# Performance work log

Hardware: AMD Instinct MI355X
Metric: run time of the kernel (lower is better)

Reference implementation:

```python
import jax, jax.numpy as jnp
import numpy as np

T, V, D = 16, 1024, 128  # number_steps, number_vectors, latent_dimension
B = 2048
EPS = 1e-12  # tf.nn.l2_normalize epsilon


def _l2_normalize(x, axis=-1):
    sq = jnp.sum(jnp.square(x), axis=axis, keepdims=True)
    return x * jax.lax.rsqrt(jnp.maximum(sq, EPS))


def setup_inputs() -> dict:
    key = jax.random.key(0)
    k1, k2, k3 = jax.random.split(key, 3)
    inputs = jax.random.normal(k1, (B, D, 1), dtype=jnp.float32)
    index = jax.random.randint(k2, (B,), 0, T, dtype=jnp.int64)
    # glorot_uniform over (T, V, D): limit = sqrt(6 / (fan_in + fan_out))
    limit = float(np.sqrt(6.0 / (V + D)))
    latent_vectors = jax.random.uniform(k3, (T, V, D), minval=-limit, maxval=limit, dtype=jnp.float32)
    return {"inputs": inputs, "latent_vectors": latent_vectors, "index": index}


def reference(inputs, latent_vectors, index):
    x = jnp.squeeze(inputs, axis=-1)                 # (B, D)
    cur = latent_vectors[index]                      # (B, V, D) gather over steps
    xn = _l2_normalize(x, axis=-1)                   # (B, D)
    ln = _l2_normalize(cur, axis=-1)                 # (B, V, D)
    sim = jnp.einsum('bvd,bd->bv', ln, xn)           # cosine similarity (B, V)
    best = jnp.argmax(sim, axis=-1)                  # (B,)
    sel = jnp.take_along_axis(cur, best[:, None, None], axis=1)  # (B, 1, D)
    return jnp.squeeze(sel, axis=1)                  # (B, D)
```

## Files before the change

### kernel.cpp

```cpp
#include <hip/hip_runtime.h>
#include <cstdint>

#define T_STEPS 16
#define V_VECS  1024
#define D_DIM   128
#define B_BATCH 2048
#define BCAP    2048

__global__ __launch_bounds__(256) void k_score(const float* __restrict__ X,
                                               const float* __restrict__ L,
                                               const int* __restrict__ idx,
                                               unsigned long long* __restrict__ partial,
                                               int* __restrict__ counts) {
    __shared__ __align__(16) float As[D_DIM][64];
    __shared__ __align__(16) float Xs[D_DIM][64];
    __shared__ float npart[4][64];
    __shared__ float invn_s[64];
    __shared__ int   blist[BCAP];
    __shared__ int   wcnt[4];

    const int t    = blockIdx.y;
    const int vt   = blockIdx.x;
    const int v0   = vt * 64;
    const int z    = blockIdx.z;
    const int tid  = threadIdx.x;
    const int lane = tid & 63;
    const int w    = tid >> 6;

    int nbase = 0;
    for (int r = 0; r < 8; ++r) {
        const int b = r * 256 + tid;
        const bool m = (idx[b] == t);
        const unsigned long long bal = __ballot(m);
        const int wpre = __popcll(bal & ((1ull << lane) - 1ull));
        if (lane == 0) wcnt[w] = __popcll(bal);
        __syncthreads();
        const int c0 = wcnt[0], c1 = wcnt[1], c2 = wcnt[2], c3 = wcnt[3];
        int base = nbase;
        if (w > 0) base += c0;
        if (w > 1) base += c1;
        if (w > 2) base += c2;
        if (m) blist[base + wpre] = b;
        nbase += c0 + c1 + c2 + c3;
        __syncthreads();
    }
    const int n = nbase;
    if (vt == 0 && z == 0 && tid == 0) counts[t] = n;
    if (z * 64 >= n) return;

    const float4* LA = (const float4*)(L + (size_t)(t * V_VECS + v0) * D_DIM);
    float ss = 0.f;
    #pragma unroll
    for (int p = 0; p < 8; ++p) {
        const int k4 = w + 4 * p;
        const float4 g = LA[lane * 32 + k4];
        As[4 * k4 + 0][lane] = g.x;
        As[4 * k4 + 1][lane] = g.y;
        As[4 * k4 + 2][lane] = g.z;
        As[4 * k4 + 3][lane] = g.w;
        ss += g.x * g.x + g.y * g.y + g.z * g.z + g.w * g.w;
    }
    npart[w][lane] = ss;
    __syncthreads();
    if (tid < 64) {
        const float s = npart[0][tid] + npart[1][tid] + npart[2][tid] + npart[3][tid];
        invn_s[tid] = rsqrtf(fmaxf(s, 1e-12f));
    }

    const int tv = tid & 15;
    const int tb = tid >> 4;
    const float4* XA = (const float4*)X;

    for (int cs = z * 64; cs < n; cs += 128) {
        __syncthreads();

        const int brow = cs + lane;
        const int bg = (brow < n) ? blist[brow] : -1;
        #pragma unroll
        for (int p = 0; p < 8; ++p) {
            const int k4 = w + 4 * p;
            float4 g = make_float4(0.f, 0.f, 0.f, 0.f);
            if (bg >= 0) g = XA[bg * 32 + k4];
            Xs[4 * k4 + 0][lane] = g.x;
            Xs[4 * k4 + 1][lane] = g.y;
            Xs[4 * k4 + 2][lane] = g.z;
            Xs[4 * k4 + 3][lane] = g.w;
        }
        __syncthreads();

        float acc[4][4] = {};
        #pragma unroll 16
        for (int k = 0; k < D_DIM; ++k) {
            const float4 av = *(const float4*)&As[k][tv * 4];
            const float4 xb = *(const float4*)&Xs[k][tb * 4];
            const float a[4] = {av.x, av.y, av.z, av.w};
            const float x[4] = {xb.x, xb.y, xb.z, xb.w};
            #pragma unroll
            for (int i = 0; i < 4; ++i)
                #pragma unroll
                for (int j = 0; j < 4; ++j)
                    acc[i][j] += a[i] * x[j];
        }

        const float invp[4] = {invn_s[tv * 4 + 0], invn_s[tv * 4 + 1],
                               invn_s[tv * 4 + 2], invn_s[tv * 4 + 3]};

        #pragma unroll
        for (int j = 0; j < 4; ++j) {
            float s = acc[0][j] * invp[0];
            int   c = v0 + tv * 4;
            #pragma unroll
            for (int i = 1; i < 4; ++i) {
                const float si = acc[i][j] * invp[i];
                const int   ci = v0 + tv * 4 + i;
                if (si > s) { s = si; c = ci; }
            }
            #pragma unroll
            for (int m = 8; m >= 1; m >>= 1) {
                const float u  = __shfl_xor(s, m);
                const int   cu = __shfl_xor(c, m);
                if (u > s || (u == s && cu < c)) { s = u; c = cu; }
            }
            if (tv == 0) {
                const int bi = cs + tb * 4 + j;
                if (bi < n) {
                    unsigned int ub = __float_as_uint(s);
                    ub = (ub & 0x80000000u) ? ~ub : (ub | 0x80000000u);
                    const unsigned long long key =
                        ((unsigned long long)ub << 32) |
                        ((unsigned long long)(unsigned)(1023 - c) << 16) |
                        (unsigned long long)(unsigned)blist[bi];
                    partial[((size_t)vt * T_STEPS + t) * BCAP + bi] = key;
                }
            }
        }
    }
}

__global__ __launch_bounds__(256) void k_gather(const float* __restrict__ L,
                                                const int* __restrict__ counts,
                                                const unsigned long long* __restrict__ partial,
                                                float* __restrict__ out) {
    __shared__ int vArr[64];
    __shared__ int bArr[64];

    const int t  = blockIdx.y;
    const int cs = blockIdx.x * 64;
    const int n  = counts[t];
    if (cs >= n) return;

    const int tid = threadIdx.x;
    const int nb  = min(64, n - cs);
    if (tid < nb) {
        const int bi = cs + tid;
        unsigned long long best = partial[(size_t)t * BCAP + bi];
        #pragma unroll
        for (int q = 1; q < 16; ++q) {
            const unsigned long long k2 =
                partial[((size_t)q * T_STEPS + t) * BCAP + bi];
            if (k2 > best) best = k2;
        }
        vArr[tid] = 1023 - (int)((best >> 16) & 0xffffull);
        bArr[tid] = (int)(best & 0xffffull);
    }
    __syncthreads();

    const int l32 = tid & 31;
    for (int q = tid >> 5; q < nb; q += 8) {
        const int b = bArr[q], v = vArr[q];
        ((float4*)out)[b * 32 + l32] =
            ((const float4*)L)[(size_t)(t * V_VECS + v) * 32 + l32];
    }
}

extern "C" void kernel_launch(void* const* d_in, const int* in_sizes, int n_in,
                              void* d_out, int out_size, void* d_ws, size_t ws_size,
                              hipStream_t stream) {
    const float* X  = (const float*)d_in[0];
    const float* L  = (const float*)d_in[1];
    const int* idx  = (const int*)d_in[2];
    float* out      = (float*)d_out;

    char* ws = (char*)d_ws;
    int* counts               = (int*)ws;
    unsigned long long* part  = (unsigned long long*)(ws + 4096);

    hipLaunchKernelGGL(k_score,  dim3(16, 16, 2), dim3(256), 0, stream,
                       X, L, idx, part, counts);
    hipLaunchKernelGGL(k_gather, dim3(32, 16),    dim3(256), 0, stream,
                       L, counts, part, out);
}
```

Measured before the change: 28.34 us.

## Shrink score kernel to single-wave blocks with 8x8 register tiles

```diff
diff --git a/kernel.cpp b/kernel.cpp
--- a/kernel.cpp
+++ b/kernel.cpp
@@ -7,122 +7,105 @@
 #define B_BATCH 2048
 #define BCAP    2048
 
-__global__ __launch_bounds__(256) void k_score(const float* __restrict__ X,
-                                               const float* __restrict__ L,
-                                               const int* __restrict__ idx,
-                                               unsigned long long* __restrict__ partial,
-                                               int* __restrict__ counts) {
+__global__ __launch_bounds__(64) void k_score(const float* __restrict__ X,
+                                              const float* __restrict__ L,
+                                              const int* __restrict__ idx,
+                                              unsigned long long* __restrict__ partial,
+                                              int* __restrict__ counts) {
     __shared__ __align__(16) float As[D_DIM][64];
     __shared__ __align__(16) float Xs[D_DIM][64];
-    __shared__ float npart[4][64];
     __shared__ float invn_s[64];
     __shared__ int   blist[BCAP];
-    __shared__ int   wcnt[4];
 
     const int t    = blockIdx.y;
     const int vt   = blockIdx.x;
     const int v0   = vt * 64;
     const int z    = blockIdx.z;
-    const int tid  = threadIdx.x;
-    const int lane = tid & 63;
-    const int w    = tid >> 6;
+    const int lane = threadIdx.x;
 
-    int nbase = 0;
-    for (int r = 0; r < 8; ++r) {
-        const int b = r * 256 + tid;
+    int n = 0;
+    for (int r = 0; r < 32; ++r) {
+        const int b = r * 64 + lane;
         const bool m = (idx[b] == t);
         const unsigned long long bal = __ballot(m);
-        const int wpre = __popcll(bal & ((1ull << lane) - 1ull));
-        if (lane == 0) wcnt[w] = __popcll(bal);
-        __syncthreads();
-        const int c0 = wcnt[0], c1 = wcnt[1], c2 = wcnt[2], c3 = wcnt[3];
-        int base = nbase;
-        if (w > 0) base += c0;
-        if (w > 1) base += c1;
-        if (w > 2) base += c2;
-        if (m) blist[base + wpre] = b;
-        nbase += c0 + c1 + c2 + c3;
-        __syncthreads();
+        if (m) blist[n + __popcll(bal & ((1ull << lane) - 1ull))] = b;
+        n += __popcll(bal);
     }
-    const int n = nbase;
-    if (vt == 0 && z == 0 && tid == 0) counts[t] = n;
+    if (vt == 0 && z == 0 && lane == 0) counts[t] = n;
     if (z * 64 >= n) return;
 
     const float4* LA = (const float4*)(L + (size_t)(t * V_VECS + v0) * D_DIM);
     float ss = 0.f;
-    #pragma unroll
-    for (int p = 0; p < 8; ++p) {
-        const int k4 = w + 4 * p;
-        const float4 g = LA[lane * 32 + k4];
-        As[4 * k4 + 0][lane] = g.x;
-        As[4 * k4 + 1][lane] = g.y;
-        As[4 * k4 + 2][lane] = g.z;
-        As[4 * k4 + 3][lane] = g.w;
+    #pragma unroll 8
+    for (int p = 0; p < 32; ++p) {
+        const float4 g = LA[lane * 32 + p];
+        As[4 * p + 0][lane] = g.x;
+        As[4 * p + 1][lane] = g.y;
+        As[4 * p + 2][lane] = g.z;
+        As[4 * p + 3][lane] = g.w;
         ss += g.x * g.x + g.y * g.y + g.z * g.z + g.w * g.w;
     }
-    npart[w][lane] = ss;
-    __syncthreads();
-    if (tid < 64) {
-        const float s = npart[0][tid] + npart[1][tid] + npart[2][tid] + npart[3][tid];
-        invn_s[tid] = rsqrtf(fmaxf(s, 1e-12f));
-    }
+    invn_s[lane] = rsqrtf(fmaxf(ss, 1e-12f));
 
-    const int tv = tid & 15;
-    const int tb = tid >> 4;
+    const int iv = lane & 7;
+    const int jb = lane >> 3;
     const float4* XA = (const float4*)X;
 
     for (int cs = z * 64; cs < n; cs += 128) {
         __syncthreads();
 
-        const int brow = cs + lane;
-        const int bg = (brow < n) ? blist[brow] : -1;
-        #pragma unroll
-        for (int p = 0; p < 8; ++p) {
-            const int k4 = w + 4 * p;
+        const int bl = cs + lane;
+        const int bg = (bl < n) ? blist[bl] : -1;
+        const float4* xr = XA + (size_t)(bg < 0 ? 0 : bg) * 32;
+        #pragma unroll 8
+        for (int p = 0; p < 32; ++p) {
             float4 g = make_float4(0.f, 0.f, 0.f, 0.f);
-            if (bg >= 0) g = XA[bg * 32 + k4];
-            Xs[4 * k4 + 0][lane] = g.x;
-            Xs[4 * k4 + 1][lane] = g.y;
-            Xs[4 * k4 + 2][lane] = g.z;
-            Xs[4 * k4 + 3][lane] = g.w;
+            if (bg >= 0) g = xr[p];
+            Xs[4 * p + 0][lane] = g.x;
+            Xs[4 * p + 1][lane] = g.y;
+            Xs[4 * p + 2][lane] = g.z;
+            Xs[4 * p + 3][lane] = g.w;
         }
         __syncthreads();
 
-        float acc[4][4] = {};
-        #pragma unroll 16
+        float acc[8][8] = {};
+        #pragma unroll 4
         for (int k = 0; k < D_DIM; ++k) {
-            const float4 av = *(const float4*)&As[k][tv * 4];
-            const float4 xb = *(const float4*)&Xs[k][tb * 4];
-            const float a[4] = {av.x, av.y, av.z, av.w};
-            const float x[4] = {xb.x, xb.y, xb.z, xb.w};
+            const float4 a0 = *(const float4*)&As[k][iv * 8];
+            const float4 a1 = *(const float4*)&As[k][iv * 8 + 4];
+            const float4 x0 = *(const float4*)&Xs[k][jb * 8];
+            const float4 x1 = *(const float4*)&Xs[k][jb * 8 + 4];
+            const float a[8] = {a0.x, a0.y, a0.z, a0.w, a1.x, a1.y, a1.z, a1.w};
+            const float x[8] = {x0.x, x0.y, x0.z, x0.w, x1.x, x1.y, x1.z, x1.w};
             #pragma unroll
-            for (int i = 0; i < 4; ++i)
+            for (int i = 0; i < 8; ++i)
                 #pragma unroll
-                for (int j = 0; j < 4; ++j)
+                for (int j = 0; j < 8; ++j)
                     acc[i][j] += a[i] * x[j];
         }
 
-        const float invp[4] = {invn_s[tv * 4 + 0], invn_s[tv * 4 + 1],
-                               invn_s[tv * 4 + 2], invn_s[tv * 4 + 3]};
+        const float4 n0 = *(const float4*)&invn_s[iv * 8];
+        const float4 n1 = *(const float4*)&invn_s[iv * 8 + 4];
+        const float inv[8] = {n0.x, n0.y, n0.z, n0.w, n1.x, n1.y, n1.z, n1.w};
 
         #pragma unroll
-        for (int j = 0; j < 4; ++j) {
-            float s = acc[0][j] * invp[0];
-            int   c = v0 + tv * 4;
+        for (int j = 0; j < 8; ++j) {
+            float s = acc[0][j] * inv[0];
+            int   c = v0 + iv * 8;
             #pragma unroll
-            for (int i = 1; i < 4; ++i) {
-                const float si = acc[i][j] * invp[i];
-                const int   ci = v0 + tv * 4 + i;
+            for (int i = 1; i < 8; ++i) {
+                const float si = acc[i][j] * inv[i];
+                const int   ci = v0 + iv * 8 + i;
                 if (si > s) { s = si; c = ci; }
             }
             #pragma unroll
-            for (int m = 8; m >= 1; m >>= 1) {
+            for (int m = 1; m <= 4; m <<= 1) {
                 const float u  = __shfl_xor(s, m);
                 const int   cu = __shfl_xor(c, m);
                 if (u > s || (u == s && cu < c)) { s = u; c = cu; }
             }
-            if (tv == 0) {
-                const int bi = cs + tb * 4 + j;
+            if (iv == 0) {
+                const int bi = cs + jb * 8 + j;
                 if (bi < n) {
                     unsigned int ub = __float_as_uint(s);
                     ub = (ub & 0x80000000u) ? ~ub : (ub | 0x80000000u);
@@ -185,7 +168,7 @@
     int* counts               = (int*)ws;
     unsigned long long* part  = (unsigned long long*)(ws + 4096);
 
-    hipLaunchKernelGGL(k_score,  dim3(16, 16, 2), dim3(256), 0, stream,
+    hipLaunchKernelGGL(k_score,  dim3(16, 16, 2), dim3(64),  0, stream,
                        X, L, idx, part, counts);
     hipLaunchKernelGGL(k_gather, dim3(32, 16),    dim3(256), 0, stream,
                        L, counts, part, out);
```

Result: slower. 50.35 us (+77.7%).

## Stream X rows from global, batch compaction sync, shrink LDS, double z-split

Applied to the files above, without the earlier changes.

```diff
diff --git a/kernel.cpp b/kernel.cpp
--- a/kernel.cpp
+++ b/kernel.cpp
@@ -7,17 +7,16 @@
 #define B_BATCH 2048
 #define BCAP    2048
 
-__global__ __launch_bounds__(256) void k_score(const float* __restrict__ X,
-                                               const float* __restrict__ L,
-                                               const int* __restrict__ idx,
-                                               unsigned long long* __restrict__ partial,
-                                               int* __restrict__ counts) {
+__global__ __launch_bounds__(256, 4) void k_score(const float* __restrict__ X,
+                                                  const float* __restrict__ L,
+                                                  const int* __restrict__ idx,
+                                                  unsigned long long* __restrict__ partial,
+                                                  int* __restrict__ counts) {
     __shared__ __align__(16) float As[D_DIM][64];
-    __shared__ __align__(16) float Xs[D_DIM][64];
     __shared__ float npart[4][64];
     __shared__ float invn_s[64];
-    __shared__ int   blist[BCAP];
-    __shared__ int   wcnt[4];
+    __shared__ unsigned short blist[BCAP];
+    __shared__ int wcnt[8][4];
 
     const int t    = blockIdx.y;
     const int vt   = blockIdx.x;
@@ -27,24 +26,29 @@
     const int lane = tid & 63;
     const int w    = tid >> 6;
 
-    int nbase = 0;
+    bool mm[8]; int wpre[8];
+    #pragma unroll
     for (int r = 0; r < 8; ++r) {
-        const int b = r * 256 + tid;
-        const bool m = (idx[b] == t);
+        const bool m = (idx[r * 256 + tid] == t);
         const unsigned long long bal = __ballot(m);
-        const int wpre = __popcll(bal & ((1ull << lane) - 1ull));
-        if (lane == 0) wcnt[w] = __popcll(bal);
-        __syncthreads();
-        const int c0 = wcnt[0], c1 = wcnt[1], c2 = wcnt[2], c3 = wcnt[3];
-        int base = nbase;
-        if (w > 0) base += c0;
-        if (w > 1) base += c1;
-        if (w > 2) base += c2;
-        if (m) blist[base + wpre] = b;
-        nbase += c0 + c1 + c2 + c3;
-        __syncthreads();
+        mm[r]   = m;
+        wpre[r] = __popcll(bal & ((1ull << lane) - 1ull));
+        if (lane == 0) wcnt[r][w] = __popcll(bal);
     }
-    const int n = nbase;
+    __syncthreads();
+    int run = 0;
+    #pragma unroll
+    for (int r = 0; r < 8; ++r) {
+        int base = run;
+        #pragma unroll
+        for (int w2 = 0; w2 < 4; ++w2) {
+            const int c = wcnt[r][w2];
+            if (w2 < w) base += c;
+            run += c;
+        }
+        if (mm[r]) blist[base + wpre[r]] = (unsigned short)(r * 256 + tid);
+    }
+    const int n = run;
     if (vt == 0 && z == 0 && tid == 0) counts[t] = n;
     if (z * 64 >= n) return;
 
@@ -71,39 +75,40 @@
     const int tb = tid >> 4;
     const float4* XA = (const float4*)X;
 
-    for (int cs = z * 64; cs < n; cs += 128) {
+    for (int cs = z * 64; cs < n; cs += 256) {
         __syncthreads();
 
-        const int brow = cs + lane;
-        const int bg = (brow < n) ? blist[brow] : -1;
-        #pragma unroll
-        for (int p = 0; p < 8; ++p) {
-            const int k4 = w + 4 * p;
-            float4 g = make_float4(0.f, 0.f, 0.f, 0.f);
-            if (bg >= 0) g = XA[bg * 32 + k4];
-            Xs[4 * k4 + 0][lane] = g.x;
-            Xs[4 * k4 + 1][lane] = g.y;
-            Xs[4 * k4 + 2][lane] = g.z;
-            Xs[4 * k4 + 3][lane] = g.w;
-        }
-        __syncthreads();
+        const int bsl = cs + tb * 4;
+        const float4* xp0 = XA + (size_t)((bsl + 0 < n) ? blist[bsl + 0] : 0) * 32;
+        const float4* xp1 = XA + (size_t)((bsl + 1 < n) ? blist[bsl + 1] : 0) * 32;
+        const float4* xp2 = XA + (size_t)((bsl + 2 < n) ? blist[bsl + 2] : 0) * 32;
+        const float4* xp3 = XA + (size_t)((bsl + 3 < n) ? blist[bsl + 3] : 0) * 32;
 
         float acc[4][4] = {};
-        #pragma unroll 16
-        for (int k = 0; k < D_DIM; ++k) {
-            const float4 av = *(const float4*)&As[k][tv * 4];
-            const float4 xb = *(const float4*)&Xs[k][tb * 4];
-            const float a[4] = {av.x, av.y, av.z, av.w};
-            const float x[4] = {xb.x, xb.y, xb.z, xb.w};
+        #pragma unroll 4
+        for (int k4 = 0; k4 < 32; ++k4) {
+            const float4 q0 = xp0[k4];
+            const float4 q1 = xp1[k4];
+            const float4 q2 = xp2[k4];
+            const float4 q3 = xp3[k4];
+            const float xk[4][4] = {{q0.x, q1.x, q2.x, q3.x},
+                                    {q0.y, q1.y, q2.y, q3.y},
+                                    {q0.z, q1.z, q2.z, q3.z},
+                                    {q0.w, q1.w, q2.w, q3.w}};
             #pragma unroll
-            for (int i = 0; i < 4; ++i)
+            for (int c = 0; c < 4; ++c) {
+                const float4 av = *(const float4*)&As[4 * k4 + c][tv * 4];
+                const float a[4] = {av.x, av.y, av.z, av.w};
                 #pragma unroll
-                for (int j = 0; j < 4; ++j)
-                    acc[i][j] += a[i] * x[j];
+                for (int i = 0; i < 4; ++i)
+                    #pragma unroll
+                    for (int j = 0; j < 4; ++j)
+                        acc[i][j] += a[i] * xk[c][j];
+            }
         }
 
-        const float invp[4] = {invn_s[tv * 4 + 0], invn_s[tv * 4 + 1],
-                               invn_s[tv * 4 + 2], invn_s[tv * 4 + 3]};
+        const float4 inv4 = *(const float4*)&invn_s[tv * 4];
+        const float invp[4] = {inv4.x, inv4.y, inv4.z, inv4.w};
 
         #pragma unroll
         for (int j = 0; j < 4; ++j) {
@@ -129,7 +134,7 @@
                     const unsigned long long key =
                         ((unsigned long long)ub << 32) |
                         ((unsigned long long)(unsigned)(1023 - c) << 16) |
-                        (unsigned long long)(unsigned)blist[bi];
+                        (unsigned long long)blist[bi];
                     partial[((size_t)vt * T_STEPS + t) * BCAP + bi] = key;
                 }
             }
@@ -185,7 +190,7 @@
     int* counts               = (int*)ws;
     unsigned long long* part  = (unsigned long long*)(ws + 4096);
 
-    hipLaunchKernelGGL(k_score,  dim3(16, 16, 2), dim3(256), 0, stream,
+    hipLaunchKernelGGL(k_score,  dim3(16, 16, 4), dim3(256), 0, stream,
                        X, L, idx, part, counts);
     hipLaunchKernelGGL(k_gather, dim3(32, 16),    dim3(256), 0, stream,
                        L, counts, part, out);
```

After: 30.61 us. +8.0%, slower.
